# Kernel tuning notes

Measured on AMD Instinct MI355X. Metric: run time of the kernel, lower is better.

Reference implementation:

```python
import jax, jax.numpy as jnp
import numpy as np

N = 50000      # nodes
E = 800000     # edges (before self-loops)
H = 6          # heads
F_IN = 64
F_OUT = 64
NEG_SLOPE = 0.2  # PyG GATv2Conv default


def setup_inputs() -> dict:
    key = jax.random.key(0)
    k1, k2, k3, k4, k5 = jax.random.split(key, 5)
    x = jax.random.normal(k1, (N, F_IN), jnp.float32)
    edge_idx = jax.random.randint(k2, (2, E), 0, N, dtype=jnp.int64)
    scale = 1.0 / np.sqrt(F_IN)
    W_l = jax.random.normal(k3, (F_IN, H * F_OUT), jnp.float32) * scale
    W_r = jax.random.normal(k4, (F_IN, H * F_OUT), jnp.float32) * scale
    att = jax.random.normal(k5, (H, F_OUT), jnp.float32) * scale
    bias = jnp.zeros((F_OUT,), jnp.float32)
    return {"x": x, "edge_idx": edge_idx, "W_l": W_l, "W_r": W_r, "att": att, "bias": bias}


def reference(x, edge_idx, W_l, W_r, att, bias):
    n = x.shape[0]
    # PyG GATv2Conv adds self-loops by default
    loops = jnp.arange(n, dtype=edge_idx.dtype)
    src = jnp.concatenate([edge_idx[0], loops])  # message sources j
    dst = jnp.concatenate([edge_idx[1], loops])  # message targets i

    gl = (x @ W_l).reshape(n, H, F_OUT)  # x_l (source-side projection)
    gr = (x @ W_r).reshape(n, H, F_OUT)  # x_r (target-side projection)

    # attention logits: a^T LeakyReLU(x_l[j] + x_r[i])  -> [Et, H]
    s = jax.nn.leaky_relu(gl[src] + gr[dst], NEG_SLOPE)
    e = jnp.einsum('ehf,hf->eh', s, att)

    # segment softmax over incoming edges of each destination node
    m = jax.ops.segment_max(e, dst, num_segments=n)          # [N, H]
    p = jnp.exp(e - m[dst])                                  # [Et, H]
    denom = jax.ops.segment_sum(p, dst, num_segments=n)     # [N, H]
    alpha = p / (denom[dst] + 1e-16)

    # weighted scatter-add of source messages
    msg = alpha[:, :, None] * gl[src]                        # [Et, H, F]
    out = jax.ops.segment_sum(msg, dst, num_segments=n)     # [N, H, F]

    # concat=False -> mean over heads, then bias, then SELU
    out = out.mean(axis=1) + bias
    return jax.nn.selu(out)
```

## Files before the change

### kernel.cpp

```cpp
#include <hip/hip_runtime.h>
#include <hip/hip_bf16.h>
#include <hip/hip_fp16.h>

typedef _Float16 half8 __attribute__((ext_vector_type(8)));
typedef _Float16 half4_t __attribute__((ext_vector_type(4)));
typedef _Float16 h2 __attribute__((ext_vector_type(2)));
typedef float f32x4 __attribute__((ext_vector_type(4)));
typedef unsigned int u32;

#define NEG_SLOPE 0.2f
#define SELU_SCALE 1.0507009873554805f
#define SELU_ALPHA 1.6732632423543772f
#define LOG2E 1.4426950408889634f
#define DEFER_THR 4.0f

#if __has_builtin(__builtin_amdgcn_fdot2)
#define FDOT2(a, b, c) __builtin_amdgcn_fdot2((a), (b), (c), false)
#else
static __device__ inline float FDOT2(h2 a, h2 b, float c) {
    return c + (float)a[0] * (float)b[0] + (float)a[1] * (float)b[1];
}
#endif

static __device__ inline h2 h2max(h2 a, h2 b) {
#if __has_builtin(__builtin_elementwise_max)
    return __builtin_elementwise_max(a, b);
#else
    h2 r; r[0] = a[0] > b[0] ? a[0] : b[0]; r[1] = a[1] > b[1] ? a[1] : b[1]; return r;
#endif
}

static __device__ inline h2 shfl_h2(h2 v, int d) {
    u32 u = __builtin_bit_cast(u32, v);
    return __builtin_bit_cast(h2, (u32)__shfl_xor((int)u, d, 64));
}

static __device__ inline float fexp2(float x) {
    float r;
    asm("v_exp_f32 %0, %1" : "=v"(r) : "v"(x));
    return r;
}

static __device__ inline h2 pk2(float a) {
#if __has_builtin(__builtin_amdgcn_cvt_pkrtz)
    return __builtin_bit_cast(h2, __builtin_amdgcn_cvt_pkrtz(a, a));
#else
    _Float16 h = (_Float16)a; return (h2){h, h};
#endif
}

__global__ __launch_bounds__(256) void gemm_kernel(
    const float* __restrict__ x, const float* __restrict__ Wl,
    const float* __restrict__ Wr, _Float16* __restrict__ glA,
    _Float16* __restrict__ glB, int n_nodes)
{
    __shared__ float xs[128 * 68];
    int row0 = blockIdx.x * 128;
    if (row0 >= n_nodes) return;

    {
        int t = threadIdx.x;
        #pragma unroll
        for (int i = 0; i < 8; i++) {
            int idx = t + i * 256;
            int r = idx >> 4, c = (idx & 15) * 4;
            int row = row0 + r;
            f32x4 v = (f32x4){0.f, 0.f, 0.f, 0.f};
            if (row < n_nodes) v = *(const f32x4*)(x + (size_t)row * 64 + c);
            *(f32x4*)(xs + r * 68 + c) = v;
        }
    }
    __syncthreads();

    int wid  = threadIdx.x >> 6;
    int lane = threadIdx.x & 63;
    int l15  = lane & 15;
    int g    = lane >> 4;
    int kb   = g * 8;
    int colbase = wid * 192;

    half8 bw0[12], bw1[12];
    #pragma unroll
    for (int t = 0; t < 12; t++) {
        int col = colbase + t * 16 + l15;
        const float* wcol = (col < 384) ? (Wl + col) : (Wr + (col - 384));
        #pragma unroll
        for (int j = 0; j < 8; j++) {
            bw0[t][j] = (_Float16)wcol[(size_t)(kb + j) * 384];
            bw1[t][j] = (_Float16)wcol[(size_t)(32 + kb + j) * 384];
        }
    }

    #pragma unroll
    for (int rt = 0; rt < 8; rt++) {
        int r0 = rt * 16;
        half8 a0, a1;
        #pragma unroll
        for (int j = 0; j < 8; j++) {
            a0[j] = (_Float16)xs[(r0 + l15) * 68 + kb + j];
            a1[j] = (_Float16)xs[(r0 + l15) * 68 + 32 + kb + j];
        }
        int nodeRow = row0 + r0 + l15;
        #pragma unroll
        for (int t = 0; t < 12; t++) {
            f32x4 acc = (f32x4){0.f, 0.f, 0.f, 0.f};
            acc = __builtin_amdgcn_mfma_f32_16x16x32_f16(bw0[t], a0, acc, 0, 0, 0);
            acc = __builtin_amdgcn_mfma_f32_16x16x32_f16(bw1[t], a1, acc, 0, 0, 0);
            if (nodeRow < n_nodes) {
                int c0 = colbase + t * 16 + g * 4;
                half4_t hv;
                #pragma unroll
                for (int r = 0; r < 4; r++) hv[r] = (_Float16)acc[r];
                _Float16* dst = (c0 < 384)
                    ? (glA + (size_t)nodeRow * 384 + c0)
                    : (glB + (size_t)nodeRow * 384 + (c0 - 384));
                *(half4_t*)dst = hv;
            }
        }
    }
}

__global__ void hist_kernel(const int* __restrict__ eidx, int* count, int n_edges) {
    int i = blockIdx.x * blockDim.x + threadIdx.x;
    if (i < n_edges) atomicAdd(&count[eidx[n_edges + i]], 1);
}

__global__ __launch_bounds__(256) void scan_local_kernel(
    const int* __restrict__ count, int* __restrict__ row_ptr,
    int* __restrict__ blksum, int* __restrict__ blockhist, int n)
{
    __shared__ int ws[4];
    __shared__ int dh[256];
    int blk = blockIdx.x, t = threadIdx.x;
    dh[t] = 0;
    __syncthreads();

    int base = blk * 1024 + t * 4;
    int d0 = (base + 0 < n) ? count[base + 0] + 1 : 0;
    int d1 = (base + 1 < n) ? count[base + 1] + 1 : 0;
    int d2 = (base + 2 < n) ? count[base + 2] + 1 : 0;
    int d3 = (base + 3 < n) ? count[base + 3] + 1 : 0;
    if (d0) atomicAdd(&dh[255 - (d0 < 255 ? d0 : 255)], 1);
    if (d1) atomicAdd(&dh[255 - (d1 < 255 ? d1 : 255)], 1);
    if (d2) atomicAdd(&dh[255 - (d2 < 255 ? d2 : 255)], 1);
    if (d3) atomicAdd(&dh[255 - (d3 < 255 ? d3 : 255)], 1);

    int tsum = d0 + d1 + d2 + d3;
    int lane = t & 63, wid = t >> 6;
    int s = tsum;
    #pragma unroll
    for (int d = 1; d < 64; d <<= 1) {
        int u = __shfl_up(s, d, 64);
        if (lane >= d) s += u;
    }
    if (lane == 63) ws[wid] = s;
    __syncthreads();
    int woff = 0;
    #pragma unroll
    for (int w = 0; w < 4; w++) if (w < wid) woff += ws[w];
    int excl = woff + s - tsum;
    if (base + 0 < n) row_ptr[base + 0] = excl;
    if (base + 1 < n) row_ptr[base + 1] = excl + d0;
    if (base + 2 < n) row_ptr[base + 2] = excl + d0 + d1;
    if (base + 3 < n) row_ptr[base + 3] = excl + d0 + d1 + d2;
    if (t == 255) blksum[blk] = woff + s;
    __syncthreads();
    blockhist[blk * 256 + t] = dh[t];
}

__global__ __launch_bounds__(256) void binscan_kernel(
    int* __restrict__ blockhist, int* __restrict__ blksum,
    int* __restrict__ row_ptr, int nblk, int n)
{
    __shared__ int ws[4];
    int b = threadIdx.x;

    if (b < 64) {
        int v = (b < nblk) ? blksum[b] : 0;
        int s = v;
        #pragma unroll
        for (int d = 1; d < 64; d <<= 1) {
            int u = __shfl_up(s, d, 64);
            if (b >= d) s += u;
        }
        if (b < nblk) blksum[b] = s - v;
        if (b == 63) row_ptr[n] = s;
    }

    int vals[64];
    #pragma unroll
    for (int blk = 0; blk < 64; blk++)
        vals[blk] = (blk < nblk) ? blockhist[blk * 256 + b] : 0;
    int run = 0;
    #pragma unroll
    for (int blk = 0; blk < 64; blk++) {
        int x = vals[blk];
        vals[blk] = run;
        run += x;
    }
    int lane = b & 63, wid = b >> 6;
    int s = run;
    #pragma unroll
    for (int d = 1; d < 64; d <<= 1) {
        int u = __shfl_up(s, d, 64);
        if (lane >= d) s += u;
    }
    if (lane == 63) ws[wid] = s;
    __syncthreads();
    int woff = 0;
    #pragma unroll
    for (int w = 0; w < 4; w++) if (w < wid) woff += ws[w];
    int basep = woff + s - run;
    #pragma unroll
    for (int blk = 0; blk < 64; blk++)
        if (blk < nblk) blockhist[blk * 256 + b] = vals[blk] + basep;
}

__global__ __launch_bounds__(256) void cursor_order_kernel(
    int* __restrict__ row_ptr, const int* __restrict__ blksum,
    const int* __restrict__ count, const int* __restrict__ blockhist,
    int* __restrict__ cursor, int* __restrict__ sorted_src,
    int* __restrict__ order, int n)
{
    __shared__ int loff[256];
    int blk = blockIdx.x, t = threadIdx.x;
    loff[t] = blockhist[blk * 256 + t];
    __syncthreads();
    int base = blk * 1024 + t * 4;
    #pragma unroll
    for (int i = 0; i < 4; i++) {
        int node = base + i;
        if (node < n) {
            int rp = row_ptr[node] + blksum[node >> 10];
            row_ptr[node] = rp;
            cursor[node] = rp + 1;
            sorted_src[rp] = node;
            int deg = count[node] + 1;
            int bin = 255 - (deg < 255 ? deg : 255);
            int pos = atomicAdd(&loff[bin], 1);
            order[pos] = node;
        }
    }
}

__global__ void scatter_kernel(const int* __restrict__ eidx, int* cursor,
                               int* sorted_src, int n_edges) {
    int i = blockIdx.x * blockDim.x + threadIdx.x;
    if (i < n_edges) {
        int d = eidx[n_edges + i];
        int s = eidx[i];
        int pos = atomicAdd(&cursor[d], 1);
        sorted_src[pos] = s;
    }
}

__global__ __launch_bounds__(256) void edge_kernel(
    const _Float16* __restrict__ glA,
    const _Float16* __restrict__ glB,
    const int* __restrict__ row_ptr,
    const int* __restrict__ sorted_src,
    const int* __restrict__ order,
    const float* __restrict__ att,
    const float* __restrict__ bias,
    float* __restrict__ out, int n_nodes)
{
    int tid  = blockIdx.x * 256 + threadIdx.x;
    int ggid = tid >> 4;
    int GG   = (gridDim.x * 256) >> 4;
    int l0  = threadIdx.x & 15;
    int oct = l0 >> 3;
    int q   = l0 & 7;
    u32 l16 = (u32)l0 * 16u;

    const char* glA_b = (const char*)glA;
    const char* glB_b = (const char*)glB;
    const _Float16 c02 = (_Float16)NEG_SLOPE;

    h2 att_h[12];
    #pragma unroll
    for (int P = 0; P < 3; P++) {
        int h = 2 * P + oct;
        f32x4 av0 = *(const f32x4*)(att + h * 64 + q * 8);
        f32x4 av1 = *(const f32x4*)(att + h * 64 + q * 8 + 4);
        att_h[P * 4 + 0] = (h2){(_Float16)(av0[0] * LOG2E), (_Float16)(av0[1] * LOG2E)};
        att_h[P * 4 + 1] = (h2){(_Float16)(av0[2] * LOG2E), (_Float16)(av0[3] * LOG2E)};
        att_h[P * 4 + 2] = (h2){(_Float16)(av1[0] * LOG2E), (_Float16)(av1[1] * LOG2E)};
        att_h[P * 4 + 3] = (h2){(_Float16)(av1[2] * LOG2E), (_Float16)(av1[3] * LOG2E)};
    }
    f32x4 bv0 = *(const f32x4*)(bias + q * 8);
    f32x4 bv1 = *(const f32x4*)(bias + q * 8 + 4);

    for (int slot = ggid; slot < n_nodes; slot += GG) {
        int node = order[slot];

        h2 gr_h[12];
        {
            u32 rbase = (u32)node * 768u;
            #pragma unroll
            for (int P = 0; P < 3; P++) {
                half8 gv = *(const half8*)(glB_b + rbase + (u32)P * 256u + l16);
                gr_h[P * 4 + 0] = ((h2*)&gv)[0];
                gr_h[P * 4 + 1] = ((h2*)&gv)[1];
                gr_h[P * 4 + 2] = ((h2*)&gv)[2];
                gr_h[P * 4 + 3] = ((h2*)&gv)[3];
            }
        }

        float m[3], sden[3];
        h2 acc[12];
        #pragma unroll
        for (int P = 0; P < 3; P++) { m[P] = -1e30f; sden[P] = 0.f; }
        #pragma unroll
        for (int j = 0; j < 12; j++) acc[j] = (h2){(_Float16)0.f, (_Float16)0.f};

        int rp = row_ptr[node], re = row_ptr[node + 1];
        int reclamp = re - 1;

        auto lsrc = [&](int idx) {
            int ii = idx < reclamp ? idx : reclamp;
            return sorted_src[ii];
        };

        half8 A0, A1, A2, B0, B1, B2;

#define LOADX(X0, X1, X2, S)                                                 \
        {                                                                    \
            u32 o = (u32)(S) * 768u + l16;                                   \
            X0 = *(const half8*)(glA_b + o);                                 \
            X1 = *(const half8*)(glA_b + o + 256);                           \
            X2 = *(const half8*)(glA_b + o + 512);                           \
        }

#define PROC1(X0, X1, X2)                                                    \
        {                                                                    \
            float e[3];                                                      \
            _Pragma("unroll")                                                \
            for (int P = 0; P < 3; P++) {                                    \
                h2 t0 = ((h2*)&X0)[0], t1 = ((h2*)&X0)[1],                   \
                   t2 = ((h2*)&X0)[2], t3 = ((h2*)&X0)[3];                   \
                if (P == 1) { t0 = ((h2*)&X1)[0]; t1 = ((h2*)&X1)[1];        \
                              t2 = ((h2*)&X1)[2]; t3 = ((h2*)&X1)[3]; }      \
                if (P == 2) { t0 = ((h2*)&X2)[0]; t1 = ((h2*)&X2)[1];        \
                              t2 = ((h2*)&X2)[2]; t3 = ((h2*)&X2)[3]; }      \
                t0 = t0 + gr_h[P * 4 + 0]; t1 = t1 + gr_h[P * 4 + 1];        \
                t2 = t2 + gr_h[P * 4 + 2]; t3 = t3 + gr_h[P * 4 + 3];        \
                t0 = h2max(t0, t0 * c02); t1 = h2max(t1, t1 * c02);          \
                t2 = h2max(t2, t2 * c02); t3 = h2max(t3, t3 * c02);          \
                e[P] = FDOT2(t3, att_h[P * 4 + 3], FDOT2(t2, att_h[P * 4 + 2],\
                       FDOT2(t1, att_h[P * 4 + 1], FDOT2(t0, att_h[P * 4 + 0],\
                       0.f))));                                              \
            }                                                                \
            _Pragma("unroll")                                                \
            for (int d = 1; d < 8; d <<= 1) {                                \
                e[0] += __shfl_xor(e[0], d, 64);                             \
                e[1] += __shfl_xor(e[1], d, 64);                             \
                e[2] += __shfl_xor(e[2], d, 64);                             \
            }                                                                \
            _Pragma("unroll")                                                \
            for (int P = 0; P < 3; P++) {                                    \
                if (e[P] > m[P] + DEFER_THR) {        \
                    float r = fexp2(m[P] - e[P]);                            \
                    sden[P] *= r;                                            \
                    h2 r2 = pk2(r);                                          \
                    acc[P * 4 + 0] = acc[P * 4 + 0] * r2;                    \
                    acc[P * 4 + 1] = acc[P * 4 + 1] * r2;                    \
                    acc[P * 4 + 2] = acc[P * 4 + 2] * r2;                    \
                    acc[P * 4 + 3] = acc[P * 4 + 3] * r2;                    \
                    m[P] = e[P];                                             \
                }                                                            \
                float p = fexp2(e[P] - m[P]);                  \
                sden[P] += p;                                                \
                h2 p2 = pk2(p);                                              \
                const h2* xv = (P == 0) ? (const h2*)&X0                     \
                             : (P == 1) ? (const h2*)&X1 : (const h2*)&X2;   \
                acc[P * 4 + 0] = acc[P * 4 + 0] + p2 * xv[0];                \
                acc[P * 4 + 1] = acc[P * 4 + 1] + p2 * xv[1];                \
                acc[P * 4 + 2] = acc[P * 4 + 2] + p2 * xv[2];                \
                acc[P * 4 + 3] = acc[P * 4 + 3] + p2 * xv[3];                \
            }                                                                \
        }

        {
            LOADX(A0, A1, A2, sorted_src[rp]);
            int sN = lsrc(rp + 1);
            int idx = rp;
            for (;;) {
                LOADX(B0, B1, B2, sN);
                int sN2 = lsrc(idx + 2);
                PROC1(A0, A1, A2);
                idx++; if (idx >= re) break;
                LOADX(A0, A1, A2, sN2);
                sN = lsrc(idx + 2);
                PROC1(B0, B1, B2);
                idx++; if (idx >= re) break;
            }
        }
#undef PROC1
#undef LOADX

        h2 iv[3];
        #pragma unroll
        for (int P = 0; P < 3; P++) {
            float inv = 1.0f / (sden[P] + 1e-16f);
            _Float16 ih = (_Float16)inv;
            iv[P] = (h2){ih, ih};
        }
        float of[8];
        #pragma unroll
        for (int j = 0; j < 4; j++) {
            h2 o = acc[0 * 4 + j] * iv[0] + acc[1 * 4 + j] * iv[1] + acc[2 * 4 + j] * iv[2];
            o = o + shfl_h2(o, 8);
            of[2 * j]     = (float)o[0];
            of[2 * j + 1] = (float)o[1];
        }

        if (l0 < 8) {
            f32x4 ov0, ov1;
            #pragma unroll
            for (int k = 0; k < 4; k++) {
                float v0 = of[k] * (1.0f / 6.0f) + bv0[k];
                float v1 = of[k + 4] * (1.0f / 6.0f) + bv1[k];
                ov0[k] = (v0 > 0.f) ? SELU_SCALE * v0
                                    : SELU_SCALE * SELU_ALPHA * (__expf(v0) - 1.0f);
                ov1[k] = (v1 > 0.f) ? SELU_SCALE * v1
                                    : SELU_SCALE * SELU_ALPHA * (__expf(v1) - 1.0f);
            }
            float* op = out + (size_t)node * 64 + q * 8;
            *(f32x4*)op = ov0;
            *(f32x4*)(op + 4) = ov1;
        }
    }
}

extern "C" void kernel_launch(void* const* d_in, const int* in_sizes, int n_in,
                              void* d_out, int out_size, void* d_ws, size_t ws_size,
                              hipStream_t stream) {
    const float* x    = (const float*)d_in[0];
    const int*   eidx = (const int*)d_in[1];
    const float* Wl   = (const float*)d_in[2];
    const float* Wr   = (const float*)d_in[3];
    const float* att  = (const float*)d_in[4];
    const float* bias = (const float*)d_in[5];
    float* out = (float*)d_out;

    int n = in_sizes[0] / 64;
    int E = in_sizes[1] / 2;
    int Et = E + n;
    int nblk = (n + 1023) / 1024;

    char* w = (char*)d_ws;
    size_t off = 0;
    auto carve = [&](size_t bytes) {
        void* p = w + off;
        off = (off + bytes + 255) & ~(size_t)255;
        return p;
    };
    _Float16* glA   = (_Float16*)carve((size_t)n * 384 * sizeof(_Float16));
    _Float16* glB   = (_Float16*)carve((size_t)n * 384 * sizeof(_Float16));
    int* count      = (int*)carve((size_t)n * sizeof(int));
    int* row_ptr    = (int*)carve((size_t)(n + 1) * sizeof(int));
    int* cursor     = (int*)carve((size_t)n * sizeof(int));
    int* sorted_src = (int*)carve((size_t)Et * sizeof(int));
    int* order      = (int*)carve((size_t)n * sizeof(int));
    int* blksum     = (int*)carve(64 * sizeof(int));
    int* blockhist  = (int*)carve((size_t)nblk * 256 * sizeof(int));
    (void)ws_size;

    int nb_e = (E + 255) / 256;

    hipMemsetAsync(count, 0, (size_t)n * sizeof(int), stream);
    hipLaunchKernelGGL(hist_kernel, dim3(nb_e), dim3(256), 0, stream, eidx, count, E);
    hipLaunchKernelGGL(scan_local_kernel, dim3(nblk), dim3(256), 0, stream,
                       count, row_ptr, blksum, blockhist, n);
    hipLaunchKernelGGL(binscan_kernel, dim3(1), dim3(256), 0, stream,
                       blockhist, blksum, row_ptr, nblk, n);
    hipLaunchKernelGGL(cursor_order_kernel, dim3(nblk), dim3(256), 0, stream,
                       row_ptr, blksum, count, blockhist, cursor, sorted_src,
                       order, n);
    hipLaunchKernelGGL(scatter_kernel, dim3(nb_e), dim3(256), 0, stream,
                       eidx, cursor, sorted_src, E);
    hipLaunchKernelGGL(gemm_kernel, dim3((n + 127) / 128), dim3(256), 0, stream,
                       x, Wl, Wr, glA, glB, n);
    hipLaunchKernelGGL(edge_kernel, dim3(2048), dim3(256), 0, stream,
                       glA, glB, row_ptr, sorted_src, order, att, bias, out, n);
}
```

Baseline: 231.3 us.

## Fuse degree histogram into GEMM launch and vectorize edge index loads

The degree-histogram work now runs in extra blocks of the projection GEMM kernel, so the two independent jobs share one launch and can overlap on the GPU. This removes one kernel launch and lets the latency-bound atomic histogram hide behind GEMM compute. Both the histogram and scatter kernels now handle four edges per thread with int4 loads, which cuts thread count and widens memory accesses. The change assumes the edge index buffer is 16-byte aligned at offset n_edges, and the GEMM blocks now run earlier in the sequence.

```diff
diff --git a/kernel.cpp b/kernel.cpp
--- a/kernel.cpp
+++ b/kernel.cpp
@@ -49,15 +49,32 @@
 #endif
 }
 
-__global__ __launch_bounds__(256) void gemm_kernel(
+__global__ __launch_bounds__(256) void gemm_hist_kernel(
     const float* __restrict__ x, const float* __restrict__ Wl,
     const float* __restrict__ Wr, _Float16* __restrict__ glA,
-    _Float16* __restrict__ glB, int n_nodes)
+    _Float16* __restrict__ glB, int n_nodes,
+    const int* __restrict__ eidx, int* __restrict__ count, int n_edges,
+    int nbG)
 {
     __shared__ float xs[128 * 68];
+    if ((int)blockIdx.x >= nbG) {
+        int i0 = ((int)blockIdx.x - nbG) * 1024 + (int)threadIdx.x * 4;
+        if (i0 + 3 < n_edges) {
+            int4 d4 = *(const int4*)(eidx + (size_t)n_edges + i0);
+            atomicAdd(&count[d4.x], 1);
+            atomicAdd(&count[d4.y], 1);
+            atomicAdd(&count[d4.z], 1);
+            atomicAdd(&count[d4.w], 1);
+        } else {
+            for (int k = 0; k < 4; k++)
+                if (i0 + k < n_edges)
+                    atomicAdd(&count[eidx[(size_t)n_edges + i0 + k]], 1);
+        }
+        return;
+    }
+
     int row0 = blockIdx.x * 128;
     if (row0 >= n_nodes) return;
-
     {
         int t = threadIdx.x;
         #pragma unroll
@@ -120,11 +137,6 @@
     }
 }
 
-__global__ void hist_kernel(const int* __restrict__ eidx, int* count, int n_edges) {
-    int i = blockIdx.x * blockDim.x + threadIdx.x;
-    if (i < n_edges) atomicAdd(&count[eidx[n_edges + i]], 1);
-}
-
 __global__ __launch_bounds__(256) void scan_local_kernel(
     const int* __restrict__ count, int* __restrict__ row_ptr,
     int* __restrict__ blksum, int* __restrict__ blockhist, int n)
@@ -243,14 +255,28 @@
     }
 }
 
-__global__ void scatter_kernel(const int* __restrict__ eidx, int* cursor,
-                               int* sorted_src, int n_edges) {
-    int i = blockIdx.x * blockDim.x + threadIdx.x;
-    if (i < n_edges) {
-        int d = eidx[n_edges + i];
-        int s = eidx[i];
-        int pos = atomicAdd(&cursor[d], 1);
-        sorted_src[pos] = s;
+__global__ __launch_bounds__(256) void scatter_kernel(
+    const int* __restrict__ eidx, int* cursor,
+    int* sorted_src, int n_edges)
+{
+    int i0 = (blockIdx.x * 256 + threadIdx.x) * 4;
+    if (i0 + 3 < n_edges) {
+        int4 s4 = *(const int4*)(eidx + i0);
+        int4 d4 = *(const int4*)(eidx + (size_t)n_edges + i0);
+        int p0 = atomicAdd(&cursor[d4.x], 1); sorted_src[p0] = s4.x;
+        int p1 = atomicAdd(&cursor[d4.y], 1); sorted_src[p1] = s4.y;
+        int p2 = atomicAdd(&cursor[d4.z], 1); sorted_src[p2] = s4.z;
+        int p3 = atomicAdd(&cursor[d4.w], 1); sorted_src[p3] = s4.w;
+    } else {
+        for (int k = 0; k < 4; k++) {
+            int i = i0 + k;
+            if (i < n_edges) {
+                int d = eidx[(size_t)n_edges + i];
+                int s = eidx[i];
+                int pos = atomicAdd(&cursor[d], 1);
+                sorted_src[pos] = s;
+            }
+        }
     }
 }
 
@@ -466,10 +492,13 @@
     int* blockhist  = (int*)carve((size_t)nblk * 256 * sizeof(int));
     (void)ws_size;
 
-    int nb_e = (E + 255) / 256;
+    int nbG = (n + 127) / 128;
+    int nbH = (E + 1023) / 1024;
+    int nbS = (E + 1023) / 1024;
 
     hipMemsetAsync(count, 0, (size_t)n * sizeof(int), stream);
-    hipLaunchKernelGGL(hist_kernel, dim3(nb_e), dim3(256), 0, stream, eidx, count, E);
+    hipLaunchKernelGGL(gemm_hist_kernel, dim3(nbG + nbH), dim3(256), 0, stream,
+                       x, Wl, Wr, glA, glB, n, eidx, count, E, nbG);
     hipLaunchKernelGGL(scan_local_kernel, dim3(nblk), dim3(256), 0, stream,
                        count, row_ptr, blksum, blockhist, n);
     hipLaunchKernelGGL(binscan_kernel, dim3(1), dim3(256), 0, stream,
@@ -477,10 +506,8 @@
     hipLaunchKernelGGL(cursor_order_kernel, dim3(nblk), dim3(256), 0, stream,
                        row_ptr, blksum, count, blockhist, cursor, sorted_src,
                        order, n);
-    hipLaunchKernelGGL(scatter_kernel, dim3(nb_e), dim3(256), 0, stream,
+    hipLaunchKernelGGL(scatter_kernel, dim3(nbS), dim3(256), 0, stream,
                        eidx, cursor, sorted_src, E);
-    hipLaunchKernelGGL(gemm_kernel, dim3((n + 127) / 128), dim3(256), 0, stream,
-                       x, Wl, Wr, glA, glB, n);
     hipLaunchKernelGGL(edge_kernel, dim3(2048), dim3(256), 0, stream,
                        glA, glB, row_ptr, sorted_src, order, att, bias, out, n);
 }
```

After: 207.7 us. 10.2% less time.
